# Kernel optimization log

Measured on AMD Instinct MI355X. Metric: run time of the kernel, lower is better.

Reference implementation:

```python
import jax, jax.numpy as jnp
import numpy as np

NUM_SEGMENTS = 100000


def setup_inputs() -> dict:
    key = jax.random.key(0)
    k1, k2 = jax.random.split(key)
    x = jax.random.normal(k1, (4000000, 32), dtype=jnp.float32)
    index = jax.random.randint(k2, (4000000,), 0, NUM_SEGMENTS, dtype=jnp.int64)
    return {"x": x, "index": index}


def reference(x, index):
    # scatter_mean(x, index, dim=0): sum rows per segment, divide by count (clamped to 1)
    sums = jax.ops.segment_sum(x, index, num_segments=NUM_SEGMENTS)  # [S, D]
    counts = jax.ops.segment_sum(jnp.ones((x.shape[0],), dtype=x.dtype), index,
                                 num_segments=NUM_SEGMENTS)  # [S]
    return sums / jnp.maximum(counts, 1.0)[:, None]
```

## Files before the change

### kernel.cpp

```cpp
#include <hip/hip_runtime.h>

#define NSEG 100000
#define DIM 32
#define NBUCKET 500
#define SEG_PER_BKT 200
#define RPB 16384
#define PTHREADS 256


__global__ void p1_block_hist(const int* __restrict__ idx,
                              int* __restrict__ blockhist,
                              int n_rows, int nblk) {
    __shared__ int hist[NBUCKET];
    int t = threadIdx.x, blk = blockIdx.x;
    for (int i = t; i < NBUCKET; i += PTHREADS) hist[i] = 0;
    __syncthreads();
    int base = blk * RPB;
    for (int it = 0; it < RPB / PTHREADS; ++it) {
        int row = base + it * PTHREADS + t;
        if (row < n_rows) {
            int b = idx[row] / SEG_PER_BKT;
            atomicAdd(&hist[b], 1);
        }
    }
    __syncthreads();
    for (int i = t; i < NBUCKET; i += PTHREADS)
        blockhist[(size_t)i * nblk + blk] = hist[i];
}

__global__ void p2_scan_blocks(int* __restrict__ blockhist,
                               int* __restrict__ totals, int nblk) {
    int bkt = blockIdx.x;
    int lane = threadIdx.x;
    int* rowp = blockhist + (size_t)bkt * nblk;
    int cpl = (nblk + 63) / 64;
    int s0 = lane * cpl;
    int s1 = min(nblk, s0 + cpl);
    int csum = 0;
    for (int i = s0; i < s1; ++i) csum += rowp[i];
    int v = csum;
    for (int d = 1; d < 64; d <<= 1) {
        int u = __shfl_up(v, d, 64);
        if (lane >= d) v += u;
    }
    int run = v - csum;
    for (int i = s0; i < s1; ++i) {
        int h = rowp[i];
        rowp[i] = run;
        run += h;
    }
    int tot = __shfl(v, 63, 64);
    if (lane == 0) totals[bkt] = tot;
}

__global__ void p3_scan_buckets(const int* __restrict__ totals,
                                int* __restrict__ bucket_base) {
    int lane = threadIdx.x;
    const int cpl = (NBUCKET + 63) / 64;
    int s0 = lane * cpl;
    int s1 = min(NBUCKET, s0 + cpl);
    int csum = 0;
    for (int i = s0; i < s1; ++i) csum += totals[i];
    int v = csum;
    for (int d = 1; d < 64; d <<= 1) {
        int u = __shfl_up(v, d, 64);
        if (lane >= d) v += u;
    }
    int run = v - csum;
    for (int i = s0; i < s1; ++i) {
        bucket_base[i] = run;
        run += totals[i];
    }
    if (lane == 63) bucket_base[NBUCKET] = v;
}

__global__ void p4_partition(const int* __restrict__ idx,
                             const int* __restrict__ blockhist,
                             const int* __restrict__ bucket_base,
                             unsigned int* __restrict__ perm,
                             int n_rows, int nblk) {
    __shared__ int cnt[NBUCKET];
    int t = threadIdx.x, blk = blockIdx.x;
    for (int i = t; i < NBUCKET; i += PTHREADS) cnt[i] = 0;
    __syncthreads();
    int base = blk * RPB;
    for (int it = 0; it < RPB / PTHREADS; ++it) {
        int row = base + it * PTHREADS + t;
        if (row < n_rows) {
            int seg = idx[row];
            int b = seg / SEG_PER_BKT;
            int rank = atomicAdd(&cnt[b], 1);
            int pos = bucket_base[b] + blockhist[(size_t)b * nblk + blk] + rank;
            perm[pos] = ((unsigned int)(seg - b * SEG_PER_BKT) << 24) |
                        (unsigned int)row;
        }
    }
}

__global__ void __launch_bounds__(1024)
p5_bucket_reduce(const float* __restrict__ x,
                 const unsigned int* __restrict__ perm,
                 const int* __restrict__ bucket_base,
                 float* __restrict__ out) {
    __shared__ float sums[SEG_PER_BKT * DIM];
    __shared__ int cnts[SEG_PER_BKT];
    int t = threadIdx.x;
    int b = blockIdx.x;
    for (int i = t; i < SEG_PER_BKT * DIM; i += 1024) sums[i] = 0.0f;
    for (int i = t; i < SEG_PER_BKT; i += 1024) cnts[i] = 0;
    __syncthreads();

    int start = bucket_base[b];
    int end   = bucket_base[b + 1];
    int hw  = t >> 5;
    int col = t & 31;

    int j = start + hw;
    for (; j + 96 < end; j += 128) {
        unsigned int p0 = perm[j];
        unsigned int p1 = perm[j + 32];
        unsigned int p2 = perm[j + 64];
        unsigned int p3 = perm[j + 96];
        float v0 = x[(size_t)(p0 & 0xFFFFFFu) * DIM + col];
        float v1 = x[(size_t)(p1 & 0xFFFFFFu) * DIM + col];
        float v2 = x[(size_t)(p2 & 0xFFFFFFu) * DIM + col];
        float v3 = x[(size_t)(p3 & 0xFFFFFFu) * DIM + col];
        atomicAdd(&sums[(p0 >> 24) * DIM + col], v0);
        atomicAdd(&sums[(p1 >> 24) * DIM + col], v1);
        atomicAdd(&sums[(p2 >> 24) * DIM + col], v2);
        atomicAdd(&sums[(p3 >> 24) * DIM + col], v3);
        if (col == 0) {
            atomicAdd(&cnts[p0 >> 24], 1);
            atomicAdd(&cnts[p1 >> 24], 1);
            atomicAdd(&cnts[p2 >> 24], 1);
            atomicAdd(&cnts[p3 >> 24], 1);
        }
    }
    for (; j < end; j += 32) {
        unsigned int p = perm[j];
        float v = x[(size_t)(p & 0xFFFFFFu) * DIM + col];
        atomicAdd(&sums[(p >> 24) * DIM + col], v);
        if (col == 0) atomicAdd(&cnts[p >> 24], 1);
    }
    __syncthreads();

    for (int e = t; e < SEG_PER_BKT * DIM; e += 1024) {
        int ls = e >> 5;
        float c = (float)cnts[ls];
        out[(size_t)b * SEG_PER_BKT * DIM + e] = sums[e] / fmaxf(c, 1.0f);
    }
}


__global__ void scatter_sum_kernel(const float* __restrict__ x,
                                   const int* __restrict__ idx,
                                   float* __restrict__ sums,
                                   float* __restrict__ cnts,
                                   int n_elems) {
    int i = blockIdx.x * blockDim.x + threadIdx.x;
    if (i >= n_elems) return;
    int row = i >> 5;
    int col = i & 31;
    int seg = idx[row];
    atomicAdd(&sums[seg * DIM + col], x[i]);
    if (col == 0) atomicAdd(&cnts[seg], 1.0f);
}

__global__ void divide_kernel(float* __restrict__ out,
                              const float* __restrict__ cnts, int n) {
    int i = blockIdx.x * blockDim.x + threadIdx.x;
    if (i >= n) return;
    float c = cnts[i >> 5];
    out[i] = out[i] / fmaxf(c, 1.0f);
}


extern "C" void kernel_launch(void* const* d_in, const int* in_sizes, int n_in,
                              void* d_out, int out_size, void* d_ws, size_t ws_size,
                              hipStream_t stream) {
    const float* x   = (const float*)d_in[0];
    const int*   idx = (const int*)d_in[1];
    float* out = (float*)d_out;

    int n_elems = in_sizes[0];
    int n_rows  = n_elems / DIM;
    int nblk    = (n_rows + RPB - 1) / RPB;

    size_t need = ((size_t)n_rows + (size_t)NBUCKET * nblk + NBUCKET + NBUCKET + 1)
                  * sizeof(int);

    if (ws_size >= need && n_rows <= (1 << 24)) {
        unsigned int* perm = (unsigned int*)d_ws;
        int* blockhist   = (int*)(perm + n_rows);
        int* totals      = blockhist + (size_t)NBUCKET * nblk;
        int* bucket_base = totals + NBUCKET;

        p1_block_hist<<<nblk, PTHREADS, 0, stream>>>(idx, blockhist, n_rows, nblk);
        p2_scan_blocks<<<NBUCKET, 64, 0, stream>>>(blockhist, totals, nblk);
        p3_scan_buckets<<<1, 64, 0, stream>>>(totals, bucket_base);
        p4_partition<<<nblk, PTHREADS, 0, stream>>>(idx, blockhist, bucket_base,
                                                    perm, n_rows, nblk);
        p5_bucket_reduce<<<NBUCKET, 1024, 0, stream>>>(x, perm, bucket_base, out);
    } else {
        float* cnts = (float*)d_ws;
        hipMemsetAsync(d_out, 0, (size_t)out_size * sizeof(float), stream);
        hipMemsetAsync(d_ws, 0, (size_t)NSEG * sizeof(float), stream);

        const int threads = 256;
        int blocks = (n_elems + threads - 1) / threads;
        scatter_sum_kernel<<<blocks, threads, 0, stream>>>(x, idx, out, cnts, n_elems);
        int blocks2 = (out_size + threads - 1) / threads;
        divide_kernel<<<blocks2, threads, 0, stream>>>(out, cnts, out_size);
    }
}
```

Baseline: 1.258 ms.

## Stage partition in LDS for coalesced writes and vectorize bucket reduction

The partition kernel now ranks each row locally, sorts the block's entries into a shared-memory buffer, and then writes them to the permutation array in bucket order, so global writes become mostly contiguous. The reduction kernel reads x as float4 with eight threads per row, pads the shared sums to stride 33 to avoid bank conflicts, and double-buffers chunks of the permutation through shared memory. Rows per partition block are halved to fit the staging buffer, which doubles the number of blocks and the size of the block histogram. Each thread now issues four LDS float atomics per row instead of one, and shared-memory use per block goes up.

```diff
diff --git a/kernel.cpp b/kernel.cpp
--- a/kernel.cpp
+++ b/kernel.cpp
@@ -4,9 +4,11 @@
 #define DIM 32
 #define NBUCKET 500
 #define SEG_PER_BKT 200
-#define RPB 16384
+#define RPB 8192
 #define PTHREADS 256
-
+#define RTHREADS 1024
+#define CHUNK 2048
+#define SUMSTRIDE 33
 
 __global__ void p1_block_hist(const int* __restrict__ idx,
                               int* __restrict__ blockhist,
@@ -16,12 +18,10 @@
     for (int i = t; i < NBUCKET; i += PTHREADS) hist[i] = 0;
     __syncthreads();
     int base = blk * RPB;
+#pragma unroll
     for (int it = 0; it < RPB / PTHREADS; ++it) {
         int row = base + it * PTHREADS + t;
-        if (row < n_rows) {
-            int b = idx[row] / SEG_PER_BKT;
-            atomicAdd(&hist[b], 1);
-        }
+        if (row < n_rows) atomicAdd(&hist[idx[row] / SEG_PER_BKT], 1);
     }
     __syncthreads();
     for (int i = t; i < NBUCKET; i += PTHREADS)
@@ -74,83 +74,173 @@
     if (lane == 63) bucket_base[NBUCKET] = v;
 }
 
-__global__ void p4_partition(const int* __restrict__ idx,
-                             const int* __restrict__ blockhist,
-                             const int* __restrict__ bucket_base,
-                             unsigned int* __restrict__ perm,
-                             int n_rows, int nblk) {
+__global__ void __launch_bounds__(PTHREADS)
+p4_partition(const int* __restrict__ idx,
+             const int* __restrict__ blockhist,
+             const int* __restrict__ bucket_base,
+             unsigned int* __restrict__ perm,
+             int n_rows, int nblk) {
+    __shared__ int scanb[NBUCKET + 1];
     __shared__ int cnt[NBUCKET];
+    __shared__ unsigned int buf[RPB];
     int t = threadIdx.x, blk = blockIdx.x;
+    int base = blk * RPB;
+    int rows_blk = min(RPB, n_rows - base);
+
     for (int i = t; i < NBUCKET; i += PTHREADS) cnt[i] = 0;
     __syncthreads();
-    int base = blk * RPB;
+
+    int segs[RPB / PTHREADS];
+#pragma unroll
     for (int it = 0; it < RPB / PTHREADS; ++it) {
-        int row = base + it * PTHREADS + t;
-        if (row < n_rows) {
-            int seg = idx[row];
+        int lr = it * PTHREADS + t;
+        int seg = -1;
+        if (lr < rows_blk) {
+            seg = idx[base + lr];
+            atomicAdd(&cnt[seg / SEG_PER_BKT], 1);
+        }
+        segs[it] = seg;
+    }
+    __syncthreads();
+
+    if (t < 64) {
+        const int cpl = (NBUCKET + 63) / 64;
+        int s0 = t * cpl, s1 = min(NBUCKET, s0 + cpl);
+        int csum = 0;
+        for (int i = s0; i < s1; ++i) csum += cnt[i];
+        int v = csum;
+        for (int d = 1; d < 64; d <<= 1) {
+            int u = __shfl_up(v, d, 64);
+            if (t >= d) v += u;
+        }
+        int run = v - csum;
+        for (int i = s0; i < s1; ++i) {
+            scanb[i] = run;
+            run += cnt[i];
+        }
+        if (t == 63) scanb[NBUCKET] = v;
+    }
+    __syncthreads();
+    for (int i = t; i < NBUCKET; i += PTHREADS) cnt[i] = 0;
+    __syncthreads();
+
+#pragma unroll
+    for (int it = 0; it < RPB / PTHREADS; ++it) {
+        int seg = segs[it];
+        if (seg >= 0) {
             int b = seg / SEG_PER_BKT;
-            int rank = atomicAdd(&cnt[b], 1);
-            int pos = bucket_base[b] + blockhist[(size_t)b * nblk + blk] + rank;
-            perm[pos] = ((unsigned int)(seg - b * SEG_PER_BKT) << 24) |
-                        (unsigned int)row;
-        }
-    }
-}
-
-__global__ void __launch_bounds__(1024)
+            int slot = scanb[b] + atomicAdd(&cnt[b], 1);
+            buf[slot] = ((unsigned int)seg << 13) |
+                        (unsigned int)(it * PTHREADS + t);
+        }
+    }
+    __syncthreads();
+
+    for (int s = t; s < rows_blk; s += PTHREADS) {
+        unsigned int e = buf[s];
+        int seg = (int)(e >> 13);
+        int lr  = (int)(e & 8191u);
+        int b   = seg / SEG_PER_BKT;
+        int ls  = seg - b * SEG_PER_BKT;
+        int gpos = bucket_base[b] + blockhist[(size_t)b * nblk + blk]
+                 + (s - scanb[b]);
+        perm[gpos] = ((unsigned int)ls << 24) | (unsigned int)(base + lr);
+    }
+}
+
+__global__ void __launch_bounds__(RTHREADS)
 p5_bucket_reduce(const float* __restrict__ x,
                  const unsigned int* __restrict__ perm,
                  const int* __restrict__ bucket_base,
                  float* __restrict__ out) {
-    __shared__ float sums[SEG_PER_BKT * DIM];
+    __shared__ float sums[SEG_PER_BKT * SUMSTRIDE];
     __shared__ int cnts[SEG_PER_BKT];
+    __shared__ unsigned int pbuf[2][CHUNK];
     int t = threadIdx.x;
     int b = blockIdx.x;
-    for (int i = t; i < SEG_PER_BKT * DIM; i += 1024) sums[i] = 0.0f;
-    for (int i = t; i < SEG_PER_BKT; i += 1024) cnts[i] = 0;
-    __syncthreads();
+    for (int i = t; i < SEG_PER_BKT * SUMSTRIDE; i += RTHREADS) sums[i] = 0.0f;
+    for (int i = t; i < SEG_PER_BKT; i += RTHREADS) cnts[i] = 0;
 
     int start = bucket_base[b];
     int end   = bucket_base[b + 1];
-    int hw  = t >> 5;
-    int col = t & 31;
-
-    int j = start + hw;
-    for (; j + 96 < end; j += 128) {
-        unsigned int p0 = perm[j];
-        unsigned int p1 = perm[j + 32];
-        unsigned int p2 = perm[j + 64];
-        unsigned int p3 = perm[j + 96];
-        float v0 = x[(size_t)(p0 & 0xFFFFFFu) * DIM + col];
-        float v1 = x[(size_t)(p1 & 0xFFFFFFu) * DIM + col];
-        float v2 = x[(size_t)(p2 & 0xFFFFFFu) * DIM + col];
-        float v3 = x[(size_t)(p3 & 0xFFFFFFu) * DIM + col];
-        atomicAdd(&sums[(p0 >> 24) * DIM + col], v0);
-        atomicAdd(&sums[(p1 >> 24) * DIM + col], v1);
-        atomicAdd(&sums[(p2 >> 24) * DIM + col], v2);
-        atomicAdd(&sums[(p3 >> 24) * DIM + col], v3);
-        if (col == 0) {
-            atomicAdd(&cnts[p0 >> 24], 1);
-            atomicAdd(&cnts[p1 >> 24], 1);
-            atomicAdd(&cnts[p2 >> 24], 1);
-            atomicAdd(&cnts[p3 >> 24], 1);
-        }
-    }
-    for (; j < end; j += 32) {
-        unsigned int p = perm[j];
-        float v = x[(size_t)(p & 0xFFFFFFu) * DIM + col];
-        atomicAdd(&sums[(p >> 24) * DIM + col], v);
-        if (col == 0) atomicAdd(&cnts[p >> 24], 1);
-    }
-    __syncthreads();
-
-    for (int e = t; e < SEG_PER_BKT * DIM; e += 1024) {
-        int ls = e >> 5;
-        float c = (float)cnts[ls];
-        out[(size_t)b * SEG_PER_BKT * DIM + e] = sums[e] / fmaxf(c, 1.0f);
-    }
-}
-
+    int total = end - start;
+
+    const float4* x4 = (const float4*)x;
+    int g   = t >> 3;
+    int sub = t & 7;
+
+    int m0 = min(CHUNK, total);
+    for (int i = t; i < m0; i += RTHREADS) pbuf[0][i] = perm[start + i];
+    __syncthreads();
+
+    int nchunks = (total + CHUNK - 1) / CHUNK;
+    for (int c = 0; c < nchunks; ++c) {
+        int cb  = start + c * CHUNK;
+        int m   = min(CHUNK, end - cb);
+        int cur = c & 1, nxt = cur ^ 1;
+
+        unsigned int r0 = 0, r1 = 0;
+        int nm = 0;
+        if (c + 1 < nchunks) {
+            int nb = cb + CHUNK;
+            nm = min(CHUNK, end - nb);
+            if (t < nm)          r0 = perm[nb + t];
+            if (t + 1024 < nm)   r1 = perm[nb + t + 1024];
+        }
+
+        int i = g;
+        for (; i + 384 < m; i += 512) {
+            unsigned int e0 = pbuf[cur][i];
+            unsigned int e1 = pbuf[cur][i + 128];
+            unsigned int e2 = pbuf[cur][i + 256];
+            unsigned int e3 = pbuf[cur][i + 384];
+            float4 v0 = x4[(size_t)(e0 & 0xFFFFFFu) * 8 + sub];
+            float4 v1 = x4[(size_t)(e1 & 0xFFFFFFu) * 8 + sub];
+            float4 v2 = x4[(size_t)(e2 & 0xFFFFFFu) * 8 + sub];
+            float4 v3 = x4[(size_t)(e3 & 0xFFFFFFu) * 8 + sub];
+            int s0 = (int)(e0 >> 24) * SUMSTRIDE + sub * 4;
+            int s1 = (int)(e1 >> 24) * SUMSTRIDE + sub * 4;
+            int s2 = (int)(e2 >> 24) * SUMSTRIDE + sub * 4;
+            int s3 = (int)(e3 >> 24) * SUMSTRIDE + sub * 4;
+            atomicAdd(&sums[s0 + 0], v0.x); atomicAdd(&sums[s0 + 1], v0.y);
+            atomicAdd(&sums[s0 + 2], v0.z); atomicAdd(&sums[s0 + 3], v0.w);
+            atomicAdd(&sums[s1 + 0], v1.x); atomicAdd(&sums[s1 + 1], v1.y);
+            atomicAdd(&sums[s1 + 2], v1.z); atomicAdd(&sums[s1 + 3], v1.w);
+            atomicAdd(&sums[s2 + 0], v2.x); atomicAdd(&sums[s2 + 1], v2.y);
+            atomicAdd(&sums[s2 + 2], v2.z); atomicAdd(&sums[s2 + 3], v2.w);
+            atomicAdd(&sums[s3 + 0], v3.x); atomicAdd(&sums[s3 + 1], v3.y);
+            atomicAdd(&sums[s3 + 2], v3.z); atomicAdd(&sums[s3 + 3], v3.w);
+            if (sub == 0) {
+                atomicAdd(&cnts[e0 >> 24], 1);
+                atomicAdd(&cnts[e1 >> 24], 1);
+                atomicAdd(&cnts[e2 >> 24], 1);
+                atomicAdd(&cnts[e3 >> 24], 1);
+            }
+        }
+        for (; i < m; i += 128) {
+            unsigned int e = pbuf[cur][i];
+            float4 v = x4[(size_t)(e & 0xFFFFFFu) * 8 + sub];
+            int s0 = (int)(e >> 24) * SUMSTRIDE + sub * 4;
+            atomicAdd(&sums[s0 + 0], v.x); atomicAdd(&sums[s0 + 1], v.y);
+            atomicAdd(&sums[s0 + 2], v.z); atomicAdd(&sums[s0 + 3], v.w);
+            if (sub == 0) atomicAdd(&cnts[e >> 24], 1);
+        }
+
+        if (c + 1 < nchunks) {
+            if (t < nm)        pbuf[nxt][t] = r0;
+            if (t + 1024 < nm) pbuf[nxt][t + 1024] = r1;
+        }
+        __syncthreads();
+    }
+
+    for (int e = t; e < SEG_PER_BKT * DIM; e += RTHREADS) {
+        int ls  = e >> 5;
+        int col = e & 31;
+        float cf = (float)cnts[ls];
+        out[(size_t)b * SEG_PER_BKT * DIM + e] =
+            sums[ls * SUMSTRIDE + col] / fmaxf(cf, 1.0f);
+    }
+}
 
 __global__ void scatter_sum_kernel(const float* __restrict__ x,
                                    const int* __restrict__ idx,
@@ -200,7 +290,7 @@
         p3_scan_buckets<<<1, 64, 0, stream>>>(totals, bucket_base);
         p4_partition<<<nblk, PTHREADS, 0, stream>>>(idx, blockhist, bucket_base,
                                                     perm, n_rows, nblk);
-        p5_bucket_reduce<<<NBUCKET, 1024, 0, stream>>>(x, perm, bucket_base, out);
+        p5_bucket_reduce<<<NBUCKET, RTHREADS, 0, stream>>>(x, perm, bucket_base, out);
     } else {
         float* cnts = (float*)d_ws;
         hipMemsetAsync(d_out, 0, (size_t)out_size * sizeof(float), stream);
```

Measured after the change: 1.229 ms. -2.3%, faster.
